# Performance work log

Hardware: AMD Instinct MI355X
Metric: run time of the kernel (lower is better)

## Reference

```python
import jax, jax.numpy as jnp
import numpy as np

B, S, DIM, NQ, NKV = 2, 2048, 4096, 32, 8
HD = DIM // NQ  # 128


def _rope(t, fc):
    # t: [B,S,H,D]; fc: [S,D/2,2] = (cos,sin). Complex multiply on (even,odd) pairs.
    b, s, h, d = t.shape
    tp = t.astype(jnp.float32).reshape(b, s, h, d // 2, 2)
    c = fc[None, :, None, :, 0]
    sn = fc[None, :, None, :, 1]
    x0, x1 = tp[..., 0], tp[..., 1]
    rot = jnp.stack([x0 * c - x1 * sn, x0 * sn + x1 * c], axis=-1)
    return rot.reshape(b, s, h, d).astype(t.dtype)


def setup_inputs() -> dict:
    key = jax.random.key(0)
    ks = jax.random.split(key, 5)
    x = jax.random.normal(ks[0], (B, S, DIM), jnp.float32)
    wq = jax.random.normal(ks[1], (DIM, NQ * HD), jnp.float32) * 0.02
    wk = jax.random.normal(ks[2], (DIM, NKV * HD), jnp.float32) * 0.02
    wv = jax.random.normal(ks[3], (DIM, NKV * HD), jnp.float32) * 0.02
    wo = jax.random.normal(ks[4], (NQ * HD, DIM), jnp.float32) * 0.02
    # Llama RoPE frequencies for positions [0, S)
    inv_freq = 1.0 / (10000.0 ** (jnp.arange(0, HD, 2, dtype=jnp.float32) / HD))
    ang = jnp.arange(S, dtype=jnp.float32)[:, None] * inv_freq[None, :]  # [S, HD/2]
    freqs_cis = jnp.stack([jnp.cos(ang), jnp.sin(ang)], axis=-1)  # [S, HD/2, 2]
    cache_key = jnp.zeros((B, S, NKV, HD), jnp.float32)
    cache_value = jnp.zeros((B, S, NKV, HD), jnp.float32)
    return {"x": x, "start_pos": 0, "freqs_cis": freqs_cis, "wq": wq, "wk": wk,
            "wv": wv, "wo": wo, "cache_key": cache_key, "cache_value": cache_value}


def reference(x, start_pos, freqs_cis, wq, wk, wv, wo, cache_key, cache_value):
    b, s, dim = x.shape
    nkv, hd = cache_key.shape[2], cache_key.shape[3]
    nq = wq.shape[1] // hd
    n_rep = nq // nkv
    xq = (x @ wq).reshape(b, s, nq, hd)
    xk = (x @ wk).reshape(b, s, nkv, hd)
    xv = (x @ wv).reshape(b, s, nkv, hd)
    xq = _rope(xq, freqs_cis)
    xk = _rope(xk, freqs_cis)
    # KV-cache write then read of the valid prefix
    ck = jax.lax.dynamic_update_slice(cache_key, xk, (0, start_pos, 0, 0))
    cv = jax.lax.dynamic_update_slice(cache_value, xv, (0, start_pos, 0, 0))
    kv_len = start_pos + s
    k = ck[:, :kv_len]
    v = cv[:, :kv_len]
    # GQA: repeat_interleave kv heads to match q heads (as original materializes)
    keys = jnp.repeat(k, n_rep, axis=2)    # [B,K,NQ,HD]
    values = jnp.repeat(v, n_rep, axis=2)
    scale = 1.0 / jnp.sqrt(jnp.float32(hd))
    scores = jnp.einsum('bqhd,bkhd->bhqk', xq, keys) * scale  # [B,H,S,K]
    attn = jax.nn.softmax(scores, axis=-1)  # NOTE: no causal mask, as in source
    out = jnp.einsum('bhqk,bkhd->bqhd', attn, values).reshape(b, s, nq * hd)
    return out @ wo
```

## Files before the change

kernel.cpp:

```cpp
#include <hip/hip_runtime.h>
#include <stdint.h>


typedef __attribute__((ext_vector_type(8))) short short8;
typedef __attribute__((ext_vector_type(4))) float f32x4;
typedef __attribute__((ext_vector_type(16))) float f32x16;

#define DEVFN static __device__ __forceinline__

DEVFN ushort f2bf(float f) {
  uint32_t u = __builtin_bit_cast(uint32_t, f);
  u += 0x7fffu + ((u >> 16) & 1);
  return (ushort)(u >> 16);
}

DEVFN void gll16(const void* g, void* l) {
  __builtin_amdgcn_global_load_lds(
      (const __attribute__((address_space(1))) void*)g,
      (__attribute__((address_space(3))) void*)l, 16, 0, 0);
}

DEVFN float xhalf_max(float v) { return fmaxf(v, __shfl_xor(v, 32)); }
DEVFN float xhalf_add(float v) { return v + __shfl_xor(v, 32); }

#if __has_builtin(__builtin_amdgcn_exp2f)
DEVFN float ex2(float x) { return __builtin_amdgcn_exp2f(x); }
#else
DEVFN float ex2(float x) {
  float r;
  asm("v_exp_f32 %0, %1" : "=v"(r) : "v"(x));
  return r;
}
#endif

DEVFN uint32_t cvtpk(float a, float b) {
  uint32_t r;
  asm("v_cvt_pk_bf16_f32 %0, %1, %2" : "=v"(r) : "v"(a), "v"(b));
  return r;
}

DEVFN float vmax16(const f32x16& v) {
  float a0 = fmaxf(fmaxf(v[0], v[1]), v[2]);
  float a1 = fmaxf(fmaxf(v[3], v[4]), v[5]);
  float a2 = fmaxf(fmaxf(v[6], v[7]), v[8]);
  float a3 = fmaxf(fmaxf(v[9], v[10]), v[11]);
  float a4 = fmaxf(fmaxf(v[12], v[13]), v[14]);
  float b0 = fmaxf(fmaxf(a0, a1), a2);
  float b1 = fmaxf(fmaxf(a3, a4), v[15]);
  return fmaxf(b0, b1);
}
DEVFN float vsum16(const f32x16& v) {
  float s0 = (v[0] + v[1]) + (v[2] + v[3]);
  float s1 = (v[4] + v[5]) + (v[6] + v[7]);
  float s2 = (v[8] + v[9]) + (v[10] + v[11]);
  float s3 = (v[12] + v[13]) + (v[14] + v[15]);
  return (s0 + s1) + (s2 + s3);
}

DEVFN short8 mk_frag(uint32_t w0, uint32_t w1, uint32_t w2, uint32_t w3, int hi) {
  uint32_t x0 = __shfl_xor(w0, 32);
  uint32_t x1 = __shfl_xor(w1, 32);
  uint32_t x2 = __shfl_xor(w2, 32);
  uint32_t x3 = __shfl_xor(w3, 32);
  uint4 u;
  u.x = hi ? x2 : w0;
  u.y = hi ? x3 : w1;
  u.z = hi ? w2 : x0;
  u.w = hi ? w3 : x1;
  return __builtin_bit_cast(short8, u);
}

#define VMW(N) asm volatile("s_waitcnt vmcnt(" #N ")" ::: "memory")

__global__ __launch_bounds__(256) void k_cvt(const float* __restrict__ src,
                                             ushort* __restrict__ dst, int n8) {
  int i = blockIdx.x * 256 + threadIdx.x;
  if (i >= n8) return;
  const float4* s4 = (const float4*)src + (size_t)i * 2;
  float4 a = s4[0], b = s4[1];
  uint4 o;
  o.x = (uint32_t)f2bf(a.x) | ((uint32_t)f2bf(a.y) << 16);
  o.y = (uint32_t)f2bf(a.z) | ((uint32_t)f2bf(a.w) << 16);
  o.z = (uint32_t)f2bf(b.x) | ((uint32_t)f2bf(b.y) << 16);
  o.w = (uint32_t)f2bf(b.z) | ((uint32_t)f2bf(b.w) << 16);
  ((uint4*)dst)[i] = o;
}

DEVFN void tr_body(const float* __restrict__ src, ushort* __restrict__ dst,
                   int R, int C, int c0, int r0, int t, ushort* tl) {
  const int r = t >> 4, c4 = (t & 15) << 2;
#pragma unroll
  for (int i = 0; i < 4; ++i) {
    const int rr = r + i * 16;
    float4 v = *(const float4*)&src[(size_t)(r0 + rr) * C + c0 + c4];
    ushort bv[4] = {f2bf(v.x), f2bf(v.y), f2bf(v.z), f2bf(v.w)};
#pragma unroll
    for (int j = 0; j < 4; ++j) {
      const int c = c4 + j;
      *(ushort*)((char*)tl + c * 128 + (((rr >> 3) ^ (c & 7)) << 4) +
                 ((rr & 7) << 1)) = bv[j];
    }
  }
  __syncthreads();
  const int cc = t >> 2;
#pragma unroll
  for (int i = 0; i < 2; ++i) {
    const int ch = (t & 3) + i * 4;
    short8 v = *(const short8*)((char*)tl + cc * 128 + ((ch ^ (cc & 7)) << 4));
    *(short8*)&dst[(size_t)(c0 + cc) * R + r0 + ch * 8] = v;
  }
}

__global__ __launch_bounds__(256) void k_tr(const float* __restrict__ src,
                                            ushort* __restrict__ dst, int R, int C) {
  __shared__ ushort tl[64 * 64];
  tr_body(src, dst, R, C, blockIdx.x * 64, blockIdx.y * 64, threadIdx.x, tl);
}

__global__ __launch_bounds__(256) void k_tr3(const float* __restrict__ wq,
                                             const float* __restrict__ wk,
                                             const float* __restrict__ wv,
                                             ushort* __restrict__ dst) {
  __shared__ ushort tl[64 * 64];
  const int bx = blockIdx.x;
  const float* src;
  ushort* d;
  int C, cb;
  if (bx < 64) { src = wq; d = dst; C = 4096; cb = bx; }
  else if (bx < 80) { src = wk; d = dst + (size_t)4096 * 4096; C = 1024; cb = bx - 64; }
  else { src = wv; d = dst + (size_t)5120 * 4096; C = 1024; cb = bx - 80; }
  tr_body(src, d, 4096, C, cb * 64, blockIdx.y * 64, threadIdx.x, tl);
}

template <int MODE>
__global__ __launch_bounds__(512, 2) void k_gemm8(
    const ushort* __restrict__ A, const ushort* __restrict__ Bp,
    const float* __restrict__ fcis, ushort* __restrict__ oQ,
    ushort* __restrict__ oK, ushort* __restrict__ oV, float* __restrict__ oC) {
  constexpr int K = 4096;
  constexpr int BN = MODE ? 256 : 192;
  constexpr int NBX = MODE ? 16 : 32;
  constexpr int ABUF = 16384;
  constexpr int BBUF = BN * 64;
  constexpr int NT = K / 32;
  constexpr int WNG = MODE ? 4 : 2;
  constexpr int MF = MODE ? 8 : 4;
  constexpr int NF = MODE ? 4 : 6;
  constexpr int MH = MF / 2;
  constexpr int MSPAN = 16 * MF;
  constexpr int NSPAN = 16 * NF;

  __shared__ char smem[4 * ABUF + 4 * BBUF];
  char* AsL = smem;
  char* BsL = smem + 4 * ABUF;

  constexpr int nwg = NBX * 16;
  const int bid = blockIdx.x;
  const int wg = (bid & 7) * (nwg >> 3) + (bid >> 3);
  const int nb = wg % NBX, mb = wg / NBX;
  const int m0 = mb * 256, n0 = nb * BN;

  const int tid = threadIdx.x;
  const int w = tid >> 6, lane = tid & 63;
  const int gg = lane >> 4, rr = lane & 15;
  const int wm = w / WNG, wn = w % WNG;

  const int l8 = lane >> 3, s7 = lane & 7;
  const int Ra0 = w * 8 + l8, Ra1 = 64 + Ra0;
  const int ea0 = s7 ^ (Ra0 & 7), ea1 = s7 ^ (Ra1 & 7);
  const ushort* agp0 = A + (size_t)(m0 + 2 * Ra0 + (ea0 >> 2)) * K + (ea0 & 3) * 8;
  const ushort* agp1 = A + (size_t)(m0 + 2 * Ra1 + (ea1 >> 2)) * K + (ea1 & 3) * 8;
  char* lda0 = AsL + w * 1024;
  char* lda1 = AsL + 8192 + w * 1024;

  const int Rb0 = w * 8 + l8;
  const int eb0 = s7 ^ (Rb0 & 7);
  const ushort* bgp0 = Bp + (size_t)(n0 + 2 * Rb0 + (eb0 >> 2)) * K + (eb0 & 3) * 8;
  char* ldb0 = BsL + w * 1024;
  const int Rb1 = MODE ? (64 + w * 8 + l8) : (64 + w * 4 + l8);
  const int eb1 = s7 ^ (Rb1 & 7);
  const ushort* bgp1 = Bp + (size_t)(n0 + 2 * Rb1 + (eb1 >> 2)) * K + (eb1 & 3) * 8;
  char* ldb1 = BsL + 8192 + (MODE ? w * 1024 : w * 512);

  auto STAGE_A = [&](int t) {
    const int bo = t & 3;
    const size_t ko = (size_t)t * 32;
    gll16(agp0 + ko, lda0 + bo * ABUF);
    gll16(agp1 + ko, lda1 + bo * ABUF);
  };
  auto STAGE_B = [&](int t) {
    const int bo = t & 3;
    const size_t ko = (size_t)t * 32;
    gll16(bgp0 + ko, ldb0 + bo * BBUF);
    if constexpr (MODE) {
      gll16(bgp1 + ko, ldb1 + bo * BBUF);
    } else {
      if (lane < 32) gll16(bgp1 + ko, ldb1 + bo * BBUF);
    }
  };

  int aoff[MF], boff[NF];
#pragma unroll
  for (int mf = 0; mf < MF; ++mf) {
    const int m = wm * MSPAN + mf * 16 + rr;
    aoff[mf] = (m >> 1) * 128 + (((((m & 1) << 2) | gg) ^ ((m >> 1) & 7)) << 4);
  }
#pragma unroll
  for (int nf = 0; nf < NF; ++nf) {
    const int n = wn * NSPAN + nf * 16 + rr;
    boff[nf] = (n >> 1) * 128 + (((((n & 1) << 2) | gg) ^ ((n >> 1) & 7)) << 4);
  }

  f32x4 acc[MF][NF] = {};
  short8 X0[MH], X1[MH], Y0[MH], Y1[MH];
  short8 Bc0[NF], Bc1[NF];

  auto RD_A = [&](int tt, short8* d, int h) {
    const char* Ab = AsL + (tt & 3) * ABUF;
#pragma unroll
    for (int i = 0; i < MH; ++i) d[i] = *(const short8*)(Ab + aoff[h * MH + i]);
  };
  auto RD_B = [&](int tt, short8* d) {
    const char* Bb = BsL + (tt & 3) * BBUF;
#pragma unroll
    for (int nf = 0; nf < NF; ++nf) d[nf] = *(const short8*)(Bb + boff[nf]);
  };
  auto MFMA_H = [&](short8* a, short8* bfr, int h) {
#pragma unroll
    for (int mi = 0; mi < MH; ++mi)
#pragma unroll
      for (int nf = 0; nf < NF; ++nf)
        acc[h + mi][nf] = __builtin_amdgcn_mfma_f32_16x16x32_bf16(
            a[mi], bfr[nf], acc[h + mi][nf], 0, 0, 0);
  };

#define GITER(T, cA0, cA1, cB, nA0, nA1, nB, STG, VN)                \
  do {                                                               \
    if constexpr (MODE == 1) RD_B((T), Bc0);                         \
    RD_A((T) + 1, nA0, 0);                                           \
    if constexpr (MODE == 0) RD_B((T) + 1, nB);                      \
    __builtin_amdgcn_sched_barrier(0);                               \
    __builtin_amdgcn_s_setprio(1);                                   \
    MFMA_H(cA0, (MODE == 1) ? Bc0 : cB, 0);                          \
    __builtin_amdgcn_s_setprio(0);                                   \
    RD_A((T) + 1, nA1, 1);                                           \
    if (STG) { STAGE_A((T) + 3); STAGE_B((T) + 3); }                 \
    __builtin_amdgcn_sched_barrier(0);                               \
    __builtin_amdgcn_s_setprio(1);                                   \
    MFMA_H(cA1, (MODE == 1) ? Bc0 : cB, MH);                         \
    __builtin_amdgcn_s_setprio(0);                                   \
    VMW(VN);                                                         \
    __builtin_amdgcn_s_barrier();                                    \
    __builtin_amdgcn_sched_barrier(0);                               \
  } while (0)

  STAGE_A(0); STAGE_B(0);
  STAGE_A(1); STAGE_B(1);
  STAGE_A(2); STAGE_B(2);
  VMW(4);
  __builtin_amdgcn_s_barrier();
  __builtin_amdgcn_sched_barrier(0);
  RD_A(0, X0, 0);
  RD_A(0, X1, 1);
  if constexpr (MODE == 0) RD_B(0, Bc0);

  for (int tp = 0; tp < 62; ++tp) {
    const int T = 2 * tp;
    GITER(T, X0, X1, Bc0, Y0, Y1, Bc1, true, 4);
    GITER(T + 1, Y0, Y1, Bc1, X0, X1, Bc0, true, 4);
  }
  GITER(124, X0, X1, Bc0, Y0, Y1, Bc1, true, 4);
  GITER(125, Y0, Y1, Bc1, X0, X1, Bc0, false, 0);
  GITER(126, X0, X1, Bc0, Y0, Y1, Bc1, false, 0);
  if constexpr (MODE == 1) RD_B(127, Bc0);
  __builtin_amdgcn_s_setprio(1);
  MFMA_H(Y0, (MODE == 1) ? Bc0 : Bc1, 0);
  MFMA_H(Y1, (MODE == 1) ? Bc0 : Bc1, MH);
  __builtin_amdgcn_s_setprio(0);
#undef GITER

  if constexpr (MODE == 1) {
#pragma unroll
    for (int mf = 0; mf < MF; ++mf) {
      const int mbase = m0 + wm * MSPAN + mf * 16 + gg * 4;
#pragma unroll
      for (int nf = 0; nf < NF; ++nf) {
        const int n = n0 + wn * NSPAN + nf * 16 + rr;
#pragma unroll
        for (int j = 0; j < 4; ++j)
          oC[(size_t)(mbase + j) * 4096 + n] = acc[mf][nf][j];
      }
    }
  } else {
    const int b = m0 >> 11;
#pragma unroll
    for (int mf = 0; mf < MF; ++mf) {
      const int mbase = m0 + wm * MSPAN + mf * 16 + gg * 4;
      const int s0 = mbase & 2047;
#pragma unroll
      for (int nf = 0; nf < NF; ++nf) {
        const int n = n0 + wn * NSPAN + nf * 16 + rr;
        if (n < 5120) {
          const int d = n & 127, ii = d >> 1;
          const float sgn = (n & 1) ? 1.0f : -1.0f;
          const float qsc = (n < 4096) ? 0.12752364599362f : 1.0f;
          ushort res[4];
#pragma unroll
          for (int j = 0; j < 4; ++j) {
            const float2 cs = ((const float2*)fcis)[(size_t)(s0 + j) * 64 + ii];
            float v = acc[mf][nf][j];
            float pv = __shfl_xor(v, 1);
            res[j] = f2bf(qsc * (v * cs.x + sgn * pv * cs.y));
          }
          if (n < 4096) {
            ushort* dst = oQ + ((size_t)(b * 32 + (n >> 7)) * 2048 + s0) * 128 + d;
#pragma unroll
            for (int j = 0; j < 4; ++j) dst[j * 128] = res[j];
          } else {
            ushort* dst =
                oK + ((size_t)(b * 8 + ((n - 4096) >> 7)) * 2048 + s0) * 128 + d;
#pragma unroll
            for (int j = 0; j < 4; ++j) dst[j * 128] = res[j];
          }
        } else {
          const int n2 = n - 5120;
          ushort4 pk;
          pk.x = f2bf(acc[mf][nf][0]);
          pk.y = f2bf(acc[mf][nf][1]);
          pk.z = f2bf(acc[mf][nf][2]);
          pk.w = f2bf(acc[mf][nf][3]);
          *(ushort4*)&oV[((size_t)(b * 8 + (n2 >> 7)) * 128 + (n2 & 127)) * 2048 + s0] =
              pk;
        }
      }
    }
  }
}

__global__ __launch_bounds__(512, 2) void k_attn(const ushort* __restrict__ Qg,
                                                 const ushort* __restrict__ Kg,
                                                 const ushort* __restrict__ Vt,
                                                 ushort* __restrict__ Og) {
  __shared__ ushort Ks[2][64 * 128];
  __shared__ ushort Vs[2][64 * 128];
  __shared__ float sml[8][32];

  const int bh = blockIdx.x, qt = blockIdx.y;
  const int b = bh >> 5, h = bh & 31, hk = h >> 2;
  const int t = threadIdx.x, w = t >> 6, lane = t & 63;
  const int ln31 = lane & 31, hi = lane >> 5;
  const int q0 = qt * 256;

  short8 qf[8];
  {
    const size_t qbase = ((size_t)bh * 2048 + q0 + w * 32 + ln31) * 128;
#pragma unroll
    for (int tt = 0; tt < 8; ++tt)
      qf[tt] = *(const short8*)&Qg[qbase + tt * 16 + hi * 8];
  }
  const size_t kgb = (size_t)(b * 8 + hk) * 2048 * 128;
  const size_t vgb = (size_t)(b * 8 + hk) * 128 * 2048;

  const int srow = t >> 3;
  const int ssl = (t & 7) * 2;
  const int s0 = ssl ^ (srow & 15);
  const int vd = 2 * (t >> 3) + ((t & 7) >> 2);
  const int vkl = (t & 3) * 16;
  const ushort* kgp = Kg + kgb + (size_t)srow * 128 + ssl * 8;
  const ushort* vgp = Vt + vgb + (size_t)vd * 2048 + vkl;

  uint4 rk0, rk1, rv0, rv1;
  auto LOAD = [&](int k0) {
    const uint4* kp = (const uint4*)(kgp + (size_t)k0 * 128);
    rk0 = kp[0];
    rk1 = kp[1];
    const uint4* vp = (const uint4*)(vgp + k0);
    rv0 = vp[0];
    rv1 = vp[1];
  };
  auto STORE = [&](int buf) {
    char* kd = (char*)Ks[buf] + srow * 256;
    *(uint4*)(kd + (s0 << 4)) = rk0;
    *(uint4*)(kd + ((s0 ^ 1) << 4)) = rk1;
    char* vdd = (char*)Vs[buf] + srow * 256;
    *(uint4*)(vdd + (s0 << 4)) = rv0;
    *(uint4*)(vdd + ((s0 ^ 1) << 4)) = rv1;
  };

  f32x16 ov[4] = {};
  float m_run = -1e30f, l_run = 0.f;

  const int mk = ln31 & 15;
  const int krb0 = ln31 * 256, krb1 = krb0 + 8192;
  const int vrb = (ln31 >> 1) * 256;
  const int vsp = (ln31 & 1) * 8 + hi;
  const int mv = ln31 >> 1;

  LOAD(0);
  STORE(0);
  __syncthreads();

  for (int tile = 0; tile < 32; ++tile) {
    const int cur = tile & 1;
    if (tile < 31) LOAD((tile + 1) * 64);

    const char* Kc = (const char*)Ks[cur];
    f32x16 p0 = {}, p1 = {};
    __builtin_amdgcn_s_setprio(1);
#pragma unroll
    for (int tt = 0; tt < 8; ++tt) {
      const int sl = ((tt * 2 + hi) ^ mk) << 4;
      short8 ka0 = *(const short8*)(Kc + krb0 + sl);
      short8 ka1 = *(const short8*)(Kc + krb1 + sl);
      p0 = __builtin_amdgcn_mfma_f32_32x32x16_bf16(ka0, qf[tt], p0, 0, 0, 0);
      p1 = __builtin_amdgcn_mfma_f32_32x32x16_bf16(ka1, qf[tt], p1, 0, 0, 0);
    }
    __builtin_amdgcn_s_setprio(0);

    const float pmax = xhalf_max(fmaxf(vmax16(p0), vmax16(p1)));
    if (!__all(pmax <= m_run + 8.0f)) {
      const float mnew = fmaxf(m_run, pmax);
      const float al = ex2(m_run - mnew);
      m_run = mnew;
      l_run *= al;
      sml[w][ln31] = al;
      const float4 a0 = *(const float4*)&sml[w][hi * 4];
      const float4 a1 = *(const float4*)&sml[w][8 + hi * 4];
      const float4 a2 = *(const float4*)&sml[w][16 + hi * 4];
      const float4 a3 = *(const float4*)&sml[w][24 + hi * 4];
      const float aa[16] = {a0.x, a0.y, a0.z, a0.w, a1.x, a1.y, a1.z, a1.w,
                            a2.x, a2.y, a2.z, a2.w, a3.x, a3.y, a3.z, a3.w};
#pragma unroll
      for (int i = 0; i < 16; ++i) {
        ov[0][i] *= aa[i]; ov[1][i] *= aa[i];
        ov[2][i] *= aa[i]; ov[3][i] *= aa[i];
      }
    }
#pragma unroll
    for (int i = 0; i < 16; ++i) p0[i] = ex2(p0[i] - m_run);
#pragma unroll
    for (int i = 0; i < 16; ++i) p1[i] = ex2(p1[i] - m_run);
    l_run += xhalf_add(vsum16(p0) + vsum16(p1));

    short8 pa[4];
    pa[0] = mk_frag(cvtpk(p0[0], p0[1]), cvtpk(p0[2], p0[3]),
                    cvtpk(p0[4], p0[5]), cvtpk(p0[6], p0[7]), hi);
    pa[1] = mk_frag(cvtpk(p0[8], p0[9]), cvtpk(p0[10], p0[11]),
                    cvtpk(p0[12], p0[13]), cvtpk(p0[14], p0[15]), hi);
    pa[2] = mk_frag(cvtpk(p1[0], p1[1]), cvtpk(p1[2], p1[3]),
                    cvtpk(p1[4], p1[5]), cvtpk(p1[6], p1[7]), hi);
    pa[3] = mk_frag(cvtpk(p1[8], p1[9]), cvtpk(p1[10], p1[11]),
                    cvtpk(p1[12], p1[13]), cvtpk(p1[14], p1[15]), hi);

    const char* Vc = (const char*)Vs[cur];
    __builtin_amdgcn_s_setprio(1);
#pragma unroll
    for (int db = 0; db < 4; ++db) {
      const int rb = vrb + db * 4096;
#pragma unroll
      for (int ks = 0; ks < 4; ++ks) {
        const int sl = ((vsp + ks * 2) ^ mv) << 4;
        short8 bv = *(const short8*)(Vc + rb + sl);
        ov[db] = __builtin_amdgcn_mfma_f32_32x32x16_bf16(pa[ks], bv, ov[db], 0, 0, 0);
      }
    }
    __builtin_amdgcn_s_setprio(0);

    if (tile < 31) STORE(cur ^ 1);
    __syncthreads();
  }

  sml[w][ln31] = l_run;
  const float4 l0 = *(const float4*)&sml[w][hi * 4];
  const float4 l1 = *(const float4*)&sml[w][8 + hi * 4];
  const float4 l2 = *(const float4*)&sml[w][16 + hi * 4];
  const float4 l3 = *(const float4*)&sml[w][24 + hi * 4];
  const float inv[16] = {1.f / l0.x, 1.f / l0.y, 1.f / l0.z, 1.f / l0.w,
                         1.f / l1.x, 1.f / l1.y, 1.f / l1.z, 1.f / l1.w,
                         1.f / l2.x, 1.f / l2.y, 1.f / l2.z, 1.f / l2.w,
                         1.f / l3.x, 1.f / l3.y, 1.f / l3.z, 1.f / l3.w};
  const int qb0 = q0 + w * 32 + hi * 4;
#pragma unroll
  for (int rg = 0; rg < 4; ++rg)
#pragma unroll
    for (int j = 0; j < 4; ++j) {
      const int sq = qb0 + rg * 8 + j;
      const size_t orow = ((size_t)(b * 2048 + sq)) * 4096 + h * 128 + ln31;
#pragma unroll
      for (int db = 0; db < 4; ++db)
        Og[orow + db * 32] = f2bf(ov[db][rg * 4 + j] * inv[rg * 4 + j]);
    }
}

extern "C" void kernel_launch(void* const* d_in, const int* in_sizes, int n_in,
                              void* d_out, int out_size, void* d_ws, size_t ws_size,
                              hipStream_t stream) {
  const float* x = (const float*)d_in[0];
  const float* fcis = (const float*)d_in[2];
  const float* wq = (const float*)d_in[3];
  const float* wk = (const float*)d_in[4];
  const float* wv = (const float*)d_in[5];
  const float* wo = (const float*)d_in[6];
  float* out = (float*)d_out;

  char* ws = (char*)d_ws;
  ushort* xb  = (ushort*)(ws);
  ushort* wsT = (ushort*)(ws + 33554432u);
  ushort* qb  = (ushort*)(ws + 83886080u);
  ushort* kb  = (ushort*)(ws + 117440512u);
  ushort* vbT = (ushort*)(ws + 125829120u);
  ushort* woT = xb;
  ushort* ao  = wsT;

  k_cvt<<<8192, 256, 0, stream>>>(x, xb, 2097152);
  k_tr3<<<dim3(96, 64), 256, 0, stream>>>(wq, wk, wv, wsT);
  k_gemm8<0><<<512, 512, 0, stream>>>(xb, wsT, fcis, qb, kb, vbT, nullptr);
  k_tr<<<dim3(64, 64), 256, 0, stream>>>(wo, woT, 4096, 4096);
  k_attn<<<dim3(64, 8), 512, 0, stream>>>(qb, kb, vbT, ao);
  k_gemm8<1><<<256, 512, 0, stream>>>(ao, woT, nullptr, nullptr, nullptr, nullptr,
                                      out);
}
```

Baseline: 525.9 us.

## Stage K/V tiles with direct global-to-LDS loads instead of register staging

```diff
diff --git a/kernel.cpp b/kernel.cpp
--- a/kernel.cpp
+++ b/kernel.cpp
@@ -361,30 +361,28 @@
   const size_t kgb = (size_t)(b * 8 + hk) * 2048 * 128;
   const size_t vgb = (size_t)(b * 8 + hk) * 128 * 2048;
 
-  const int srow = t >> 3;
-  const int ssl = (t & 7) * 2;
-  const int s0 = ssl ^ (srow & 15);
-  const int vd = 2 * (t >> 3) + ((t & 7) >> 2);
-  const int vkl = (t & 3) * 16;
-  const ushort* kgp = Kg + kgb + (size_t)srow * 128 + ssl * 8;
-  const ushort* vgp = Vt + vgb + (size_t)vd * 2048 + vkl;
-
-  uint4 rk0, rk1, rv0, rv1;
-  auto LOAD = [&](int k0) {
-    const uint4* kp = (const uint4*)(kgp + (size_t)k0 * 128);
-    rk0 = kp[0];
-    rk1 = kp[1];
-    const uint4* vp = (const uint4*)(vgp + k0);
-    rv0 = vp[0];
-    rv1 = vp[1];
-  };
-  auto STORE = [&](int buf) {
-    char* kd = (char*)Ks[buf] + srow * 256;
-    *(uint4*)(kd + (s0 << 4)) = rk0;
-    *(uint4*)(kd + ((s0 ^ 1) << 4)) = rk1;
-    char* vdd = (char*)Vs[buf] + srow * 256;
-    *(uint4*)(vdd + (s0 << 4)) = rv0;
-    *(uint4*)(vdd + ((s0 ^ 1) << 4)) = rv1;
+  const int kr1 = t >> 4, ks1 = t & 15;
+  const int kr2 = 32 + kr1;
+  const ushort* kq1 = Kg + kgb + (size_t)kr1 * 128 + ((ks1 ^ (kr1 & 15)) << 3);
+  const ushort* kq2 = Kg + kgb + (size_t)kr2 * 128 + ((ks1 ^ (kr2 & 15)) << 3);
+  const int vR1 = t >> 4, vR2 = 32 + vR1;
+  const int vsi1 = ks1 ^ (vR1 & 15), vsi2 = ks1 ^ (vR2 & 15);
+  const ushort* vq1 = Vt + vgb +
+      (size_t)((vR1 >> 4) * 32 + 2 * (vR1 & 15) + (vsi1 >> 3)) * 2048 +
+      ((vsi1 >> 1) & 3) * 16 + (vsi1 & 1) * 8;
+  const ushort* vq2 = Vt + vgb +
+      (size_t)((vR2 >> 4) * 32 + 2 * (vR2 & 15) + (vsi2 >> 3)) * 2048 +
+      ((vsi2 >> 1) & 3) * 16 + (vsi2 & 1) * 8;
+  char* kld = (char*)Ks[0] + w * 1024;
+  char* vld = (char*)Vs[0] + w * 1024;
+
+  auto STAGE = [&](int tile, int buf) {
+    const size_t kko = (size_t)tile * 8192;
+    const size_t vko = (size_t)tile * 64;
+    gll16(kq1 + kko, kld + buf * 16384);
+    gll16(kq2 + kko, kld + buf * 16384 + 8192);
+    gll16(vq1 + vko, vld + buf * 16384);
+    gll16(vq2 + vko, vld + buf * 16384 + 8192);
   };
 
   f32x16 ov[4] = {};
@@ -396,13 +394,14 @@
   const int vsp = (ln31 & 1) * 8 + hi;
   const int mv = ln31 >> 1;
 
-  LOAD(0);
-  STORE(0);
-  __syncthreads();
+  STAGE(0, 0);
+  VMW(0);
+  __builtin_amdgcn_s_barrier();
+  __builtin_amdgcn_sched_barrier(0);
 
   for (int tile = 0; tile < 32; ++tile) {
     const int cur = tile & 1;
-    if (tile < 31) LOAD((tile + 1) * 64);
+    if (tile < 31) STAGE(tile + 1, cur ^ 1);
 
     const char* Kc = (const char*)Ks[cur];
     f32x16 p0 = {}, p1 = {};
@@ -466,8 +465,11 @@
     }
     __builtin_amdgcn_s_setprio(0);
 
-    if (tile < 31) STORE(cur ^ 1);
-    __syncthreads();
+    if (tile < 31) {
+      VMW(0);
+      __builtin_amdgcn_s_barrier();
+      __builtin_amdgcn_sched_barrier(0);
+    }
   }
 
   sml[w][ln31] = l_run;
```

Result: slower. 536.8 us (+2.1%).
